# Optimization experiments

Measured on AMD Instinct MI355X. Metric: run time of the kernel, lower is better.

Reference implementation:

```python
import jax, jax.numpy as jnp
import numpy as np

B = 4096
OBS_DIM = 1024
E_OUT = 512
H1 = 2048
H2 = 2048


def setup_inputs() -> dict:
    key = jax.random.key(0)
    ks = jax.random.split(key, 12)
    def kaiming(k, shape, fan_in):
        return jax.random.normal(k, shape, dtype=jnp.float32) * np.float32(np.sqrt(2.0 / fan_in))
    obs = jax.random.normal(ks[0], (B, OBS_DIM), dtype=jnp.float32)
    # lineare: Linear(obs_dim, e_outputs), torch weight shape [out, in]
    We = kaiming(ks[1], (E_OUT, OBS_DIM), OBS_DIM)
    be = jax.random.normal(ks[2], (E_OUT,), dtype=jnp.float32) * 0.01
    # obs_dim attention heads, each Linear(e_outputs, 2), stacked
    attn_W = kaiming(ks[3], (OBS_DIM, E_OUT, 2), E_OUT)
    attn_b = jax.random.normal(ks[4], (OBS_DIM, 2), dtype=jnp.float32) * 0.01
    # v_net: Linear(obs_dim,H1)+tanh, Linear(H1,H2)+[dropout(eval:no-op)]+tanh, Linear(H2,1)
    W1 = kaiming(ks[5], (H1, OBS_DIM), OBS_DIM)
    b1 = jnp.zeros((H1,), dtype=jnp.float32)
    W2 = kaiming(ks[6], (H2, H1), H1)
    b2 = jnp.zeros((H2,), dtype=jnp.float32)
    W3 = kaiming(ks[7], (1, H2), H2)
    b3 = jnp.zeros((1,), dtype=jnp.float32)
    return {"obs": obs, "We": We, "be": be, "attn_W": attn_W, "attn_b": attn_b,
            "W1": W1, "b1": b1, "W2": W2, "b2": b2, "W3": W3, "b3": b3}


def reference(obs, We, be, attn_W, attn_b, W1, b1, W2, b2, W3, b3):
    # e = tanh(lineare(obs)) : [B, E_OUT]
    e = jnp.tanh(obs @ We.T + be)
    # all obs_dim attention heads batched into one contraction: [B, OBS_DIM, 2]
    logits = jnp.einsum('be,oec->boc', e, attn_W) + attn_b
    # softmax over the 2 logits, keep prob of class 1 -> Attention [B, OBS_DIM]
    attention = jax.nn.softmax(logits, axis=-1)[..., 1]
    state_attention = obs * attention
    # v_net (eval mode: dropout is identity)
    h = jnp.tanh(state_attention @ W1.T + b1)
    h = jnp.tanh(h @ W2.T + b2)
    v = jnp.squeeze(h @ W3.T + b3, -1)  # [B]
    return (v, attention)
```

## Files before the change

kernel.cpp:

```cpp
#include <hip/hip_runtime.h>
#include <hip/hip_bf16.h>

typedef unsigned short u16;
typedef u16 u16x4 __attribute__((ext_vector_type(4)));
typedef u16 u16x8 __attribute__((ext_vector_type(8)));
typedef __bf16 bf16x8 __attribute__((ext_vector_type(8)));
typedef float f32x4 __attribute__((ext_vector_type(4)));

__device__ __forceinline__ u16 f2bf(float f) {
  unsigned u = __float_as_uint(f);
  u += 0x7FFFu + ((u >> 16) & 1u);
  return (u16)(u >> 16);
}
__device__ __forceinline__ float bf2f(u16 h) {
  return __uint_as_float(((unsigned)h) << 16);
}
__device__ __forceinline__ float tanh_fast(float x) {
  float t = __expf(2.0f * x);
  return 1.0f - 2.0f / (t + 1.0f);
}
__device__ __forceinline__ float sigmoid_fast(float x) {
  return 1.0f / (1.0f + __expf(-x));
}

__device__ __forceinline__ void glds16(const u16* g, u16* l) {
  __builtin_amdgcn_global_load_lds(
      (const __attribute__((address_space(1))) unsigned int*)g,
      (__attribute__((address_space(3))) unsigned int*)l, 16, 0, 0);
}

__device__ __forceinline__ void cvt4(const float* __restrict__ s, u16* __restrict__ d, int q) {
  float4 v = ((const float4*)s)[q];
  u16x4 o = { f2bf(v.x), f2bf(v.y), f2bf(v.z), f2bf(v.w) };
  ((u16x4*)d)[q] = o;
}

__global__ __launch_bounds__(256)
void prep_kernel(const float* __restrict__ obs, const float* __restrict__ We,
                 const float* __restrict__ W1, const float* __restrict__ W2,
                 const float* __restrict__ aW, const float* __restrict__ ab,
                 u16* __restrict__ obs_b, u16* __restrict__ We_b,
                 u16* __restrict__ W1_b, u16* __restrict__ W2_b,
                 u16* __restrict__ Wd, float* __restrict__ bd,
                 float* __restrict__ vzero) {
  int q = blockIdx.x * 256 + threadIdx.x;
  if (q < 1024) ((float4*)vzero)[q] = (float4){0.f, 0.f, 0.f, 0.f};
  if (q < 1048576) { cvt4(obs, obs_b, q); return; }
  q -= 1048576;
  if (q < 131072) { cvt4(We, We_b, q); return; }
  q -= 131072;
  if (q < 524288) { cvt4(W1, W1_b, q); return; }
  q -= 524288;
  if (q < 1048576) { cvt4(W2, W2_b, q); return; }
  q -= 1048576;
  if (q < 131072) {
    int i0 = q * 4;
    int o = i0 >> 9, e0 = i0 & 511;
    const float* p = aW + (size_t)o * 1024 + e0 * 2;
    float4 v0 = *(const float4*)p;
    float4 v1 = *(const float4*)(p + 4);
    u16x4 od = { f2bf(v0.y - v0.x), f2bf(v0.w - v0.z),
                 f2bf(v1.y - v1.x), f2bf(v1.w - v1.z) };
    *(u16x4*)(Wd + i0) = od;
    if (q < 256) {
      float4 a0 = *(const float4*)(ab + q * 8);
      float4 a1 = *(const float4*)(ab + q * 8 + 4);
      float4 ob = { a0.y - a0.x, a0.w - a0.z, a1.y - a1.x, a1.w - a1.z };
      *(float4*)(bd + q * 4) = ob;
    }
  }
}

template <int BM, int BN, int EP>
__global__ __launch_bounds__(256, 2)
void gemm_bt(const u16* __restrict__ A, const u16* __restrict__ Bt,
             int N, int K,
             const float* __restrict__ bias,
             u16* __restrict__ outb, float* __restrict__ outf,
             const u16* __restrict__ obsb, u16* __restrict__ sa) {
  constexpr int CA = BM / 32;
  constexpr int CB = BN / 32;
  constexpr int MI = BM / 32;
  constexpr int NJ = BN / 32;

  __shared__ __align__(16) u16 As0[BM * 64];
  __shared__ __align__(16) u16 Bs0[BN * 64];
  __shared__ __align__(16) u16 As1[BM * 64];
  __shared__ __align__(16) u16 Bs1[BN * 64];

  const int tid = threadIdx.x;
  const int lane = tid & 63;
  const int wave = tid >> 6;
  const int bm = blockIdx.x, bn = blockIdx.y;

  const int r0 = tid >> 3;
  const int kcs = ((tid & 7) ^ (r0 & 7)) * 8;

  const u16* gA = A + (size_t)(bm * BM + r0) * K + kcs;
  const u16* gB = Bt + (size_t)(bn * BN + r0) * K + kcs;

  const int wm = (wave >> 1) * (BM / 2);
  const int wn = (wave & 1) * (BN / 2);
  const int fr = lane & 15;
  const int hi = lane >> 4;
  const int frx = fr & 7;

  f32x4 acc[MI][NJ];
#pragma unroll
  for (int i = 0; i < MI; ++i)
#pragma unroll
    for (int j = 0; j < NJ; ++j)
      acc[i][j] = (f32x4){0.f, 0.f, 0.f, 0.f};

  auto stage = [&](u16* __restrict__ dA, u16* __restrict__ dB) {
#pragma unroll
    for (int q = 0; q < CA; ++q)
      glds16(gA + (size_t)q * 32 * K, dA + tid * 8 + q * 2048);
#pragma unroll
    for (int q = 0; q < CB; ++q)
      glds16(gB + (size_t)q * 32 * K, dB + tid * 8 + q * 2048);
    gA += 64; gB += 64;
  };

  auto compute = [&](const u16* sA, const u16* sB) {
#pragma unroll
    for (int s = 0; s < 2; ++s) {
      const int ck = ((s * 4 + hi) ^ frx) * 8;
      bf16x8 a[MI], b[NJ];
#pragma unroll
      for (int i = 0; i < MI; ++i)
        a[i] = *(const bf16x8*)(sA + (wm + i * 16 + fr) * 64 + ck);
#pragma unroll
      for (int j = 0; j < NJ; ++j)
        b[j] = *(const bf16x8*)(sB + (wn + j * 16 + fr) * 64 + ck);
#pragma unroll
      for (int i = 0; i < MI; ++i)
#pragma unroll
        for (int j = 0; j < NJ; ++j)
          acc[i][j] = __builtin_amdgcn_mfma_f32_16x16x32_bf16(a[i], b[j], acc[i][j], 0, 0, 0);
    }
  };

  const int T = K >> 6;
  stage(As0, Bs0);
  __syncthreads();
  for (int k = 0; k < T; k += 2) {
    stage(As1, Bs1);
    compute(As0, Bs0);
    __syncthreads();
    if (k + 2 < T) stage(As0, Bs0);
    compute(As1, Bs1);
    __syncthreads();
  }

#pragma unroll
  for (int j = 0; j < NJ; ++j) {
    const int col = bn * BN + wn + j * 16 + fr;
    const float bv = bias[col];
#pragma unroll
    for (int i = 0; i < MI; ++i) {
#pragma unroll
      for (int r = 0; r < 4; ++r) {
        const int row = bm * BM + wm + i * 16 + hi * 4 + r;
        const float x = acc[i][j][r] + bv;
        const size_t idx = (size_t)row * N + col;
        if constexpr (EP == 0) {
          outb[idx] = f2bf(tanh_fast(x));
        } else {
          const float att = sigmoid_fast(x);
          outf[idx] = att;
          sa[idx] = f2bf(bf2f(obsb[idx]) * att);
        }
      }
    }
  }
}

template <int EP>
__global__ __launch_bounds__(512, 1)
void gemm_big(const u16* __restrict__ A, const u16* __restrict__ Bt,
              int N, int K,
              const float* __restrict__ bias,
              u16* __restrict__ outb,
              const float* __restrict__ W3, const float* __restrict__ b3,
              float* __restrict__ vout) {
  constexpr int MI = 4;
  constexpr int NJ = 2;

  __shared__ __align__(16) u16 As0[8192], Bs0[8192];
  __shared__ __align__(16) u16 As1[8192], Bs1[8192];
  __shared__ __align__(16) u16 As2[8192], Bs2[8192];
  __shared__ __align__(16) u16 As3[8192], Bs3[8192];

  const int tid = threadIdx.x;
  const int lane = tid & 63;
  const int wave = tid >> 6;
  const int bm = blockIdx.x, bn = blockIdx.y;

  const int r0 = tid >> 3;
  const int kcs = ((tid & 7) ^ (r0 & 7)) * 8;

  const u16* gA0 = A + (size_t)(bm * 128 + r0) * K + kcs;
  const u16* gA1 = gA0 + (size_t)64 * K;
  const u16* gB0 = Bt + (size_t)(bn * 128 + r0) * K + kcs;
  const u16* gB1 = gB0 + (size_t)64 * K;

  const int wm = (wave >> 2) * 64;
  const int wn = (wave & 3) * 32;
  const int fr = lane & 15;
  const int hi = lane >> 4;
  const int frx = fr & 7;

  f32x4 acc[MI][NJ];
#pragma unroll
  for (int i = 0; i < MI; ++i)
#pragma unroll
    for (int j = 0; j < NJ; ++j)
      acc[i][j] = (f32x4){0.f, 0.f, 0.f, 0.f};

  const int T = K >> 6;

  auto stage = [&](int ts, u16* __restrict__ dA, u16* __restrict__ dB) {
    const size_t o = (size_t)ts * 64;
    glds16(gA0 + o, dA + tid * 8);
    glds16(gA1 + o, dA + 4096 + tid * 8);
    glds16(gB0 + o, dB + tid * 8);
    glds16(gB1 + o, dB + 4096 + tid * 8);
  };

  auto compute = [&](const u16* sA, const u16* sB) {
#pragma unroll
    for (int s = 0; s < 2; ++s) {
      const int ck = ((s * 4 + hi) ^ frx) * 8;
      bf16x8 a[MI], b[NJ];
#pragma unroll
      for (int j = 0; j < NJ; ++j)
        b[j] = *(const bf16x8*)(sB + (wn + j * 16 + fr) * 64 + ck);
#pragma unroll
      for (int i = 0; i < MI; ++i)
        a[i] = *(const bf16x8*)(sA + (wm + i * 16 + fr) * 64 + ck);
      __builtin_amdgcn_s_setprio(1);
#pragma unroll
      for (int i = 0; i < MI; ++i)
#pragma unroll
        for (int j = 0; j < NJ; ++j)
          acc[i][j] = __builtin_amdgcn_mfma_f32_16x16x32_bf16(a[i], b[j], acc[i][j], 0, 0, 0);
      __builtin_amdgcn_s_setprio(0);
    }
  };

  stage(0, As0, Bs0);
  stage(1, As1, Bs1);
  stage(2, As2, Bs2);

#define SLOT(t, Ac, Bc, Asg, Bsg)                                   \
  do {                                                              \
    asm volatile("s_waitcnt vmcnt(8)" ::: "memory");                \
    __builtin_amdgcn_sched_barrier(0);                              \
    __builtin_amdgcn_s_barrier();                                   \
    __builtin_amdgcn_sched_barrier(0);                              \
    {                                                               \
      int ts = (t) + 3; if (ts > T - 1) ts = T - 1;                 \
      stage(ts, Asg, Bsg);                                          \
    }                                                               \
    compute(Ac, Bc);                                                \
  } while (0)

  for (int m = 0; m < T; m += 4) {
    SLOT(m + 0, As0, Bs0, As3, Bs3);
    SLOT(m + 1, As1, Bs1, As0, Bs0);
    SLOT(m + 2, As2, Bs2, As1, Bs1);
    SLOT(m + 3, As3, Bs3, As2, Bs2);
  }
#undef SLOT

  asm volatile("s_waitcnt vmcnt(0)" ::: "memory");

  if constexpr (EP == 2) {
    float vpart[MI][4];
#pragma unroll
    for (int i = 0; i < MI; ++i)
#pragma unroll
      for (int r = 0; r < 4; ++r) vpart[i][r] = 0.f;
#pragma unroll
    for (int j = 0; j < NJ; ++j) {
      const int col = bn * 128 + wn + j * 16 + fr;
      const float bv = bias[col];
      const float w3 = W3[col];
#pragma unroll
      for (int i = 0; i < MI; ++i)
#pragma unroll
        for (int r = 0; r < 4; ++r)
          vpart[i][r] += tanh_fast(acc[i][j][r] + bv) * w3;
    }
    const bool lead = (fr == 0);
    const bool addb = (bn == 0) && ((wave & 3) == 0);
#pragma unroll
    for (int i = 0; i < MI; ++i)
#pragma unroll
      for (int r = 0; r < 4; ++r) {
        float p = vpart[i][r];
        p += __shfl_xor(p, 8);
        p += __shfl_xor(p, 4);
        p += __shfl_xor(p, 2);
        p += __shfl_xor(p, 1);
        if (lead) {
          const int row = bm * 128 + wm + i * 16 + hi * 4 + r;
          atomicAdd(vout + row, addb ? p + b3[0] : p);
        }
      }
  } else {
#pragma unroll
    for (int j = 0; j < NJ; ++j) {
      const int col = bn * 128 + wn + j * 16 + fr;
      const float bv = bias[col];
#pragma unroll
      for (int i = 0; i < MI; ++i) {
#pragma unroll
        for (int r = 0; r < 4; ++r) {
          const int row = bm * 128 + wm + i * 16 + hi * 4 + r;
          outb[(size_t)row * N + col] = f2bf(tanh_fast(acc[i][j][r] + bv));
        }
      }
    }
  }
}

extern "C" void kernel_launch(void* const* d_in, const int* in_sizes, int n_in,
                              void* d_out, int out_size, void* d_ws, size_t ws_size,
                              hipStream_t stream) {
  const float* obs   = (const float*)d_in[0];
  const float* We    = (const float*)d_in[1];
  const float* be    = (const float*)d_in[2];
  const float* attnW = (const float*)d_in[3];
  const float* attnb = (const float*)d_in[4];
  const float* W1    = (const float*)d_in[5];
  const float* b1    = (const float*)d_in[6];
  const float* W2    = (const float*)d_in[7];
  const float* b2    = (const float*)d_in[8];
  const float* W3    = (const float*)d_in[9];
  const float* b3    = (const float*)d_in[10];
  float* out = (float*)d_out;

  char* ws = (char*)d_ws;
  u16*   We_b  = (u16*)(ws + 0x00000000);
  u16*   Wd_b  = (u16*)(ws + 0x00100000);
  u16*   W1_b  = (u16*)(ws + 0x00200000);
  u16*   W2_b  = (u16*)(ws + 0x00600000);
  float* bd    = (float*)(ws + 0x00E00000);
  u16*   obs_b = (u16*)(ws + 0x00E01000);
  u16*   e_b   = (u16*)(ws + 0x01601000);
  u16*   sa_b  = (u16*)(ws + 0x01A01000);
  u16*   h1_b  = (u16*)(ws + 0x02201000);

  prep_kernel<<<11264, 256, 0, stream>>>(obs, We, W1, W2, attnW, attnb,
                                         obs_b, We_b, W1_b, W2_b, Wd_b, bd, out);

  gemm_bt<64, 64, 0><<<dim3(64, 8), 256, 0, stream>>>(
      obs_b, We_b, 512, 1024, be, e_b, nullptr, nullptr, nullptr);
  gemm_bt<128, 64, 1><<<dim3(32, 16), 256, 0, stream>>>(
      e_b, Wd_b, 1024, 512, bd, nullptr, out + 4096, obs_b, sa_b);
  gemm_big<0><<<dim3(32, 16), 512, 0, stream>>>(
      sa_b, W1_b, 2048, 1024, b1, h1_b, nullptr, nullptr, nullptr);
  gemm_big<2><<<dim3(32, 16), 512, 0, stream>>>(
      h1_b, W2_b, 2048, 2048, b2, nullptr, W3, b3, out);
}
```

Before: 206.2 us.

## Replace 4-stage 128x128 big GEMM with 256x128 tile, double-buffered 4-wave kernel

The two large v_net GEMMs move from 128x128 tiles on 8 waves with a 4-deep async LDS pipeline to 256x128 tiles on 4 waves. Each wave now owns a 128x64 sub-tile with 32 MFMA accumulators, which raises arithmetic intensity per LDS load. The LDS pipeline is cut to simple double buffering with __syncthreads, and the setprio hints are removed. The grid halves to 256 blocks, one per CU, which risks exposing more memory latency and lowering occupancy. Register pressure also rises.

```diff
diff --git a/kernel.cpp b/kernel.cpp
--- a/kernel.cpp
+++ b/kernel.cpp
@@ -177,20 +177,21 @@
 }
 
 template <int EP>
-__global__ __launch_bounds__(512, 1)
-void gemm_big(const u16* __restrict__ A, const u16* __restrict__ Bt,
-              int N, int K,
-              const float* __restrict__ bias,
-              u16* __restrict__ outb,
-              const float* __restrict__ W3, const float* __restrict__ b3,
-              float* __restrict__ vout) {
-  constexpr int MI = 4;
-  constexpr int NJ = 2;
-
-  __shared__ __align__(16) u16 As0[8192], Bs0[8192];
-  __shared__ __align__(16) u16 As1[8192], Bs1[8192];
-  __shared__ __align__(16) u16 As2[8192], Bs2[8192];
-  __shared__ __align__(16) u16 As3[8192], Bs3[8192];
+__global__ __launch_bounds__(256, 1)
+void gemm_wide(const u16* __restrict__ A, const u16* __restrict__ Bt,
+               int N, int K,
+               const float* __restrict__ bias,
+               u16* __restrict__ outb,
+               const float* __restrict__ W3, const float* __restrict__ b3,
+               float* __restrict__ vout) {
+  constexpr int BM = 256, BN = 128;
+  constexpr int MI = 8;
+  constexpr int NJ = 4;
+
+  __shared__ __align__(16) u16 As0[BM * 64];
+  __shared__ __align__(16) u16 Bs0[BN * 64];
+  __shared__ __align__(16) u16 As1[BM * 64];
+  __shared__ __align__(16) u16 Bs1[BN * 64];
 
   const int tid = threadIdx.x;
   const int lane = tid & 63;
@@ -200,13 +201,11 @@
   const int r0 = tid >> 3;
   const int kcs = ((tid & 7) ^ (r0 & 7)) * 8;
 
-  const u16* gA0 = A + (size_t)(bm * 128 + r0) * K + kcs;
-  const u16* gA1 = gA0 + (size_t)64 * K;
-  const u16* gB0 = Bt + (size_t)(bn * 128 + r0) * K + kcs;
-  const u16* gB1 = gB0 + (size_t)64 * K;
-
-  const int wm = (wave >> 2) * 64;
-  const int wn = (wave & 3) * 32;
+  const u16* gA = A + (size_t)(bm * BM + r0) * K + kcs;
+  const u16* gB = Bt + (size_t)(bn * BN + r0) * K + kcs;
+
+  const int wm = (wave >> 1) * 128;
+  const int wn = (wave & 1) * 64;
   const int fr = lane & 15;
   const int hi = lane >> 4;
   const int frx = fr & 7;
@@ -218,14 +217,14 @@
     for (int j = 0; j < NJ; ++j)
       acc[i][j] = (f32x4){0.f, 0.f, 0.f, 0.f};
 
-  const int T = K >> 6;
-
-  auto stage = [&](int ts, u16* __restrict__ dA, u16* __restrict__ dB) {
-    const size_t o = (size_t)ts * 64;
-    glds16(gA0 + o, dA + tid * 8);
-    glds16(gA1 + o, dA + 4096 + tid * 8);
-    glds16(gB0 + o, dB + tid * 8);
-    glds16(gB1 + o, dB + 4096 + tid * 8);
+  auto stage = [&](u16* __restrict__ dA, u16* __restrict__ dB) {
+#pragma unroll
+    for (int q = 0; q < 8; ++q)
+      glds16(gA + (size_t)q * 32 * K, dA + tid * 8 + q * 2048);
+#pragma unroll
+    for (int q = 0; q < 4; ++q)
+      glds16(gB + (size_t)q * 32 * K, dB + tid * 8 + q * 2048);
+    gA += 64; gB += 64;
   };
 
   auto compute = [&](const u16* sA, const u16* sB) {
@@ -239,42 +238,25 @@
 #pragma unroll
       for (int i = 0; i < MI; ++i)
         a[i] = *(const bf16x8*)(sA + (wm + i * 16 + fr) * 64 + ck);
-      __builtin_amdgcn_s_setprio(1);
 #pragma unroll
       for (int i = 0; i < MI; ++i)
 #pragma unroll
         for (int j = 0; j < NJ; ++j)
           acc[i][j] = __builtin_amdgcn_mfma_f32_16x16x32_bf16(a[i], b[j], acc[i][j], 0, 0, 0);
-      __builtin_amdgcn_s_setprio(0);
     }
   };
 
-  stage(0, As0, Bs0);
-  stage(1, As1, Bs1);
-  stage(2, As2, Bs2);
-
-#define SLOT(t, Ac, Bc, Asg, Bsg)                                   \
-  do {                                                              \
-    asm volatile("s_waitcnt vmcnt(8)" ::: "memory");                \
-    __builtin_amdgcn_sched_barrier(0);                              \
-    __builtin_amdgcn_s_barrier();                                   \
-    __builtin_amdgcn_sched_barrier(0);                              \
-    {                                                               \
-      int ts = (t) + 3; if (ts > T - 1) ts = T - 1;                 \
-      stage(ts, Asg, Bsg);                                          \
-    }                                                               \
-    compute(Ac, Bc);                                                \
-  } while (0)
-
-  for (int m = 0; m < T; m += 4) {
-    SLOT(m + 0, As0, Bs0, As3, Bs3);
-    SLOT(m + 1, As1, Bs1, As0, Bs0);
-    SLOT(m + 2, As2, Bs2, As1, Bs1);
-    SLOT(m + 3, As3, Bs3, As2, Bs2);
-  }
-#undef SLOT
-
-  asm volatile("s_waitcnt vmcnt(0)" ::: "memory");
+  const int T = K >> 6;
+  stage(As0, Bs0);
+  __syncthreads();
+  for (int k = 0; k < T; k += 2) {
+    stage(As1, Bs1);
+    compute(As0, Bs0);
+    __syncthreads();
+    if (k + 2 < T) stage(As0, Bs0);
+    compute(As1, Bs1);
+    __syncthreads();
+  }
 
   if constexpr (EP == 2) {
     float vpart[MI][4];
@@ -284,7 +266,7 @@
       for (int r = 0; r < 4; ++r) vpart[i][r] = 0.f;
 #pragma unroll
     for (int j = 0; j < NJ; ++j) {
-      const int col = bn * 128 + wn + j * 16 + fr;
+      const int col = bn * BN + wn + j * 16 + fr;
       const float bv = bias[col];
       const float w3 = W3[col];
 #pragma unroll
@@ -294,7 +276,7 @@
           vpart[i][r] += tanh_fast(acc[i][j][r] + bv) * w3;
     }
     const bool lead = (fr == 0);
-    const bool addb = (bn == 0) && ((wave & 3) == 0);
+    const bool addb = (bn == 0) && ((wave & 1) == 0);
 #pragma unroll
     for (int i = 0; i < MI; ++i)
 #pragma unroll
@@ -305,20 +287,20 @@
         p += __shfl_xor(p, 2);
         p += __shfl_xor(p, 1);
         if (lead) {
-          const int row = bm * 128 + wm + i * 16 + hi * 4 + r;
+          const int row = bm * BM + wm + i * 16 + hi * 4 + r;
           atomicAdd(vout + row, addb ? p + b3[0] : p);
         }
       }
   } else {
 #pragma unroll
     for (int j = 0; j < NJ; ++j) {
-      const int col = bn * 128 + wn + j * 16 + fr;
+      const int col = bn * BN + wn + j * 16 + fr;
       const float bv = bias[col];
 #pragma unroll
       for (int i = 0; i < MI; ++i) {
 #pragma unroll
         for (int r = 0; r < 4; ++r) {
-          const int row = bm * 128 + wm + i * 16 + hi * 4 + r;
+          const int row = bm * BM + wm + i * 16 + hi * 4 + r;
           outb[(size_t)row * N + col] = f2bf(tanh_fast(acc[i][j][r] + bv));
         }
       }
@@ -360,8 +342,8 @@
       obs_b, We_b, 512, 1024, be, e_b, nullptr, nullptr, nullptr);
   gemm_bt<128, 64, 1><<<dim3(32, 16), 256, 0, stream>>>(
       e_b, Wd_b, 1024, 512, bd, nullptr, out + 4096, obs_b, sa_b);
-  gemm_big<0><<<dim3(32, 16), 512, 0, stream>>>(
+  gemm_wide<0><<<dim3(16, 16), 256, 0, stream>>>(
       sa_b, W1_b, 2048, 1024, b1, h1_b, nullptr, nullptr, nullptr);
-  gemm_big<2><<<dim3(32, 16), 512, 0, stream>>>(
+  gemm_wide<2><<<dim3(16, 16), 256, 0, stream>>>(
       h1_b, W2_b, 2048, 2048, b2, nullptr, W3, b3, out);
 }
```

Result: slower. 217.1 us (+5.3%).
